# Kernel tuning notes

Measured on AMD Instinct MI355X. Metric: run time of the kernel, lower is better.

## Reference

```python
import jax, jax.numpy as jnp
import numpy as np

IN_DIM = 128
HID = 128
OUT = 128

def _linear(x, W, b):
    return x @ W + b

def setup_inputs() -> dict:
    key = jax.random.key(0)
    ks = jax.random.split(key, 16)
    B, N = 2, 512
    def w(k, fan_in, fan_out):
        lim = 1.0 / np.sqrt(fan_in)
        return jax.random.uniform(k, (fan_in, fan_out), jnp.float32, -lim, lim)
    def bvec(k, fan_in, fan_out):
        lim = 1.0 / np.sqrt(fan_in)
        return jax.random.uniform(k, (fan_out,), jnp.float32, -lim, lim)
    return {
        "features": jax.random.normal(ks[0], (B, N, IN_DIM), jnp.float32),
        "coords": jax.random.normal(ks[1], (B, N, 3), jnp.float32),
        "eW1": w(ks[2], 2 * IN_DIM + 1, HID), "eb1": bvec(ks[3], 2 * IN_DIM + 1, HID),
        "eW2": w(ks[4], HID, HID), "eb2": bvec(ks[5], HID, HID),
        "nW1": w(ks[6], IN_DIM + HID, HID), "nb1": bvec(ks[7], IN_DIM + HID, HID),
        "nW2": w(ks[8], HID, OUT), "nb2": bvec(ks[9], HID, OUT),
        "cW1": w(ks[10], HID, HID), "cb1": bvec(ks[11], HID, HID),
        "cW2": w(ks[12], HID, 1), "cb2": bvec(ks[13], HID, 1),
    }

def reference(features, coords, eW1, eb1, eW2, eb2, nW1, nb1, nW2, nb2, cW1, cb1, cW2, cb2):
    B, N, D = features.shape
    # pairwise coordinate differences and distances: (B, N, N, 3), (B, N, N, 1)
    coord_diff = coords[:, :, None, :] - coords[:, None, :, :]
    distances = jnp.sqrt(jnp.sum(coord_diff ** 2, axis=-1, keepdims=True) + 1e-8)
    # all-pairs edge features: (B, N, N, 2D+1)
    feat_i = jnp.broadcast_to(features[:, :, None, :], (B, N, N, D))
    feat_j = jnp.broadcast_to(features[:, None, :, :], (B, N, N, D))
    edge_features = jnp.concatenate([feat_i, feat_j, distances], axis=-1)
    edge_hidden = _linear(jax.nn.silu(_linear(edge_features, eW1, eb1)), eW2, eb2)
    # mean over neighbors j -> (B, N, HID)
    aggregated = jnp.mean(edge_hidden, axis=2)
    node_input = jnp.concatenate([features, aggregated], axis=-1)
    updated_features = _linear(jax.nn.silu(_linear(node_input, nW1, nb1)), nW2, nb2)
    # coordinate update
    coord_weights = _linear(jax.nn.silu(_linear(edge_hidden, cW1, cb1)), cW2, cb2)  # (B,N,N,1)
    updated_coords = coords + jnp.mean(coord_weights * coord_diff, axis=2)
    return (updated_features, updated_coords)
```

## Files before the change

kernel.cpp:

```cpp
#include <hip/hip_runtime.h>
#include <hip/hip_bf16.h>
#include <math.h>


typedef float f32x4 __attribute__((ext_vector_type(4)));
typedef short short8 __attribute__((ext_vector_type(8)));

#define MFMA16(a, b, c) __builtin_amdgcn_mfma_f32_16x16x32_bf16((a), (b), (c), 0, 0, 0)

__device__ __forceinline__ short f2bf(float x) {
    __hip_bfloat16 h = __float2bfloat16(x);
    union { __hip_bfloat16 h; short s; } v; v.h = h;
    return v.s;
}
__device__ __forceinline__ float bf2f(short s) {
    union { unsigned u; float f; } v; v.u = ((unsigned)(unsigned short)s) << 16;
    return v.f;
}
__device__ __forceinline__ float silu_f(float x) {
    return x * __builtin_amdgcn_rcpf(1.0f + __expf(-x));
}

__device__ __forceinline__ int swz(int row, int col) {
    int byte = (row << 8) | (col << 1);
    byte ^= (row & 7) << 4;
    return byte >> 1;
}

__global__ void egnn_prew(const float* __restrict__ feat, const float* __restrict__ eW1,
                          const float* __restrict__ eb1,
                          const float* __restrict__ eW2, const float* __restrict__ cW1,
                          const float* __restrict__ eb2, const float* __restrict__ cb1,
                          float* __restrict__ Abuf, float* __restrict__ Bbuf,
                          unsigned short* __restrict__ MbfT, float* __restrict__ bias2ws) {
    const int bid = blockIdx.x;
    const int t = threadIdx.x;
    if (bid < 1024) {
        __shared__ float f[128];
        if (t < 128) f[t] = feat[bid * 128 + t];
        __syncthreads();
        const int col  = t & 127;
        const int half = t >> 7;
        const float* W = eW1 + (size_t)half * 128 * 128 + col;
        float acc = half ? 0.f : eb1[col];
        #pragma unroll 8
        for (int k = 0; k < 128; ++k) acc += f[k] * W[(size_t)k * 128];
        if (half == 0) Abuf[bid * 128 + col] = acc;
        else           Bbuf[bid * 128 + col] = acc;
    } else {
        const int idx = (bid - 1024) * 2 + (t >> 7);
        const int c = t & 127;
        if (idx < 128) {
            float acc = 0.f;
            #pragma unroll 8
            for (int h = 0; h < 128; ++h) acc += eW2[idx * 128 + h] * cW1[h * 128 + c];
            MbfT[c * 128 + idx] = (unsigned short)f2bf(acc);
        } else if (idx == 128) {
            float acc = cb1[c];
            #pragma unroll 8
            for (int h = 0; h < 128; ++h) acc += eb2[h] * cW1[h * 128 + c];
            bias2ws[c] = acc;
        }
    }
}

__global__ void __launch_bounds__(512) egnn_main(
    const float* __restrict__ features, const float* __restrict__ coords,
    const float* __restrict__ eW1, const float* __restrict__ eW2,
    const float* __restrict__ eb2,
    const float* __restrict__ nW1, const float* __restrict__ nb1,
    const float* __restrict__ nW2, const float* __restrict__ nb2,
    const float* __restrict__ cW2, const float* __restrict__ cb2,
    const float* __restrict__ Abuf, const float* __restrict__ Bbuf,
    const unsigned short* __restrict__ MbfT, const float* __restrict__ bias2ws,
    float* __restrict__ out_feat, float* __restrict__ out_coord)
{
    constexpr int Nn = 512;
    __shared__ __align__(16) short se[128 * 128];
    __shared__ __align__(16) float dynbuf[1792];
    __shared__ float aw[128], wd[128];
    __shared__ float aggs[128], aggh[128], hbuf[128];
    __shared__ float cred[8][3];
    __shared__ float ci3[3];

    float (*cdp)[3][128]  = reinterpret_cast<float(*)[3][128]>(dynbuf);
    float (*warr)[4][128] = reinterpret_cast<float(*)[4][128]>(dynbuf + 768);
    float (*aggred)[128]  = reinterpret_cast<float(*)[128]>(se);
    float (*part)[128]    = reinterpret_cast<float(*)[128]>(dynbuf);
    float* pfi = dynbuf + 512;

    const int tid  = threadIdx.x;
    const int lane = tid & 63;
    const int wave = tid >> 6;
    const int node = blockIdx.x;
    const int b    = node >> 9;

    if (tid < 128) {
        aw[tid] = Abuf[node * 128 + tid];
        wd[tid] = eW1[256 * 128 + tid];
    }
    if (tid == 0) {
        ci3[0] = coords[node * 3 + 0];
        ci3[1] = coords[node * 3 + 1];
        ci3[2] = coords[node * 3 + 2];
    }

    const int r0 = (wave >> 2) * 64;
    const int c0 = (wave & 3) * 32;
    const int cfrag = c0 + (lane & 15);
    const int koff  = (lane >> 4) * 8;

    short8 wfM[2][4];
    #pragma unroll
    for (int n2 = 0; n2 < 2; ++n2)
        #pragma unroll
        for (int k = 0; k < 4; ++k)
            wfM[n2][k] = *(const short8*)&MbfT[(size_t)(cfrag + n2 * 16) * 128 + k * 32 + koff];
    __syncthreads();

    const float b2_0  = bias2ws[cfrag], b2_1 = bias2ws[cfrag + 16];
    const float cw2_0 = cW2[cfrag],     cw2_1 = cW2[cfrag + 16];
    const float cb2v  = cb2[0];
    const float cix = ci3[0], ciy = ci3[1], ciz = ci3[2];

    const int jr = tid >> 2, cb = (tid & 3) * 32;
    const int rg = tid >> 4, c8 = (tid & 15) * 8;

    float ap[8];
    #pragma unroll
    for (int q = 0; q < 8; ++q) ap[q] = 0.f;
    float cax = 0.f, cay = 0.f, caz = 0.f;

    for (int t = 0; t < 4; ++t) {
        const int par = t & 1;
        {
            const int j = t * 128 + jr;
            const float dx = cix - coords[(b * Nn + j) * 3 + 0];
            const float dy = ciy - coords[(b * Nn + j) * 3 + 1];
            const float dz = ciz - coords[(b * Nn + j) * 3 + 2];
            const float dj = sqrtf(dx * dx + dy * dy + dz * dz + 1e-8f);
            if ((tid & 3) == 0) {
                cdp[par][0][jr] = dx; cdp[par][1][jr] = dy; cdp[par][2][jr] = dz;
            }
            const float* Bj = Bbuf + (size_t)(b * Nn + j) * 128 + cb;
            #pragma unroll
            for (int cc = 0; cc < 32; cc += 8) {
                f32x4 x0 = *(const f32x4*)(Bj + cc);
                f32x4 x1 = *(const f32x4*)(Bj + cc + 4);
                short8 v;
                #pragma unroll
                for (int r = 0; r < 4; ++r) {
                    const int c = cb + cc + r;
                    v[r] = f2bf(silu_f(aw[c] + x0[r] + dj * wd[c]));
                }
                #pragma unroll
                for (int r = 0; r < 4; ++r) {
                    const int c = cb + cc + 4 + r;
                    v[4 + r] = f2bf(silu_f(aw[c] + x1[r] + dj * wd[c]));
                }
                *(short8*)&se[swz(jr, cb + cc)] = v;
            }
        }
        __syncthreads();

        f32x4 acc[4][2];
        #pragma unroll
        for (int m = 0; m < 4; ++m) {
            acc[m][0] = (f32x4){b2_0, b2_0, b2_0, b2_0};
            acc[m][1] = (f32x4){b2_1, b2_1, b2_1, b2_1};
        }
        #pragma unroll
        for (int m = 0; m < 4; ++m)
            #pragma unroll
            for (int k = 0; k < 4; ++k) {
                short8 a = *(const short8*)&se[swz(r0 + m * 16 + (lane & 15), k * 32 + koff)];
                acc[m][0] = MFMA16(a, wfM[0][k], acc[m][0]);
                acc[m][1] = MFMA16(a, wfM[1][k], acc[m][1]);
            }

        #pragma unroll
        for (int r = 0; r < 4; ++r) {
            short8 v = *(const short8*)&se[swz(rg * 4 + r, c8)];
            #pragma unroll
            for (int q = 0; q < 8; ++q) ap[q] += bf2f(v[q]);
        }

        #pragma unroll
        for (int m = 0; m < 4; ++m)
            #pragma unroll
            for (int reg = 0; reg < 4; ++reg) {
                float v = silu_f(acc[m][0][reg]) * cw2_0
                        + silu_f(acc[m][1][reg]) * cw2_1;
                v += __shfl_xor(v, 1); v += __shfl_xor(v, 2);
                v += __shfl_xor(v, 4); v += __shfl_xor(v, 8);
                if ((lane & 15) == 0)
                    warr[par][wave & 3][r0 + m * 16 + (lane >> 4) * 4 + reg] = v;
            }
        __syncthreads();

        if (lane < 16) {
            const int row = wave * 16 + lane;
            const float w = warr[par][0][row] + warr[par][1][row]
                          + warr[par][2][row] + warr[par][3][row] + cb2v;
            cax += w * cdp[par][0][row];
            cay += w * cdp[par][1][row];
            caz += w * cdp[par][2][row];
        }
    }

    #pragma unroll
    for (int q = 0; q < 8; ++q) aggred[rg][c8 + q] = ap[q];
    {
        float sx = cax, sy = cay, sz = caz;
        sx += __shfl_xor(sx, 1); sy += __shfl_xor(sy, 1); sz += __shfl_xor(sz, 1);
        sx += __shfl_xor(sx, 2); sy += __shfl_xor(sy, 2); sz += __shfl_xor(sz, 2);
        sx += __shfl_xor(sx, 4); sy += __shfl_xor(sy, 4); sz += __shfl_xor(sz, 4);
        sx += __shfl_xor(sx, 8); sy += __shfl_xor(sy, 8); sz += __shfl_xor(sz, 8);
        if (lane == 0) { cred[wave][0] = sx; cred[wave][1] = sy; cred[wave][2] = sz; }
    }
    __syncthreads();

    const int c = tid & 127, g = tid >> 7;
    if (tid < 128) {
        float s = 0.f;
        #pragma unroll
        for (int gg = 0; gg < 32; ++gg) s += aggred[gg][tid];
        aggs[tid] = s;
        pfi[tid]  = features[node * 128 + tid];
    }
    if (tid < 3) {
        float s = 0.f;
        #pragma unroll
        for (int w = 0; w < 8; ++w) s += cred[w][tid];
        out_coord[node * 3 + tid] = ci3[tid] + s * (1.f / 512.f);
    }
    __syncthreads();

    {
        float a2 = 0.f;
        #pragma unroll 8
        for (int k = g * 32; k < g * 32 + 32; ++k) a2 += aggs[k] * eW2[k * 128 + c];
        if (g) part[g][c] = a2;
        __syncthreads();
        if (!g) aggh[c] = (a2 + part[1][c] + part[2][c] + part[3][c]) * (1.f / 512.f) + eb2[c];
        __syncthreads();
    }
    {
        float a2 = (g == 0) ? nb1[c] : 0.f;
        if (g < 2) {
            #pragma unroll 8
            for (int k = g * 64; k < g * 64 + 64; ++k) a2 += pfi[k] * nW1[k * 128 + c];
        } else {
            #pragma unroll 8
            for (int k = (g - 2) * 64; k < (g - 2) * 64 + 64; ++k)
                a2 += aggh[k] * nW1[(128 + k) * 128 + c];
        }
        if (g) part[g][c] = a2;
        __syncthreads();
        if (!g) hbuf[c] = silu_f(a2 + part[1][c] + part[2][c] + part[3][c]);
        __syncthreads();
    }
    {
        float a2 = (g == 0) ? nb2[c] : 0.f;
        #pragma unroll 8
        for (int k = g * 32; k < g * 32 + 32; ++k) a2 += hbuf[k] * nW2[k * 128 + c];
        if (g) part[g][c] = a2;
        __syncthreads();
        if (!g) out_feat[node * 128 + c] = a2 + part[1][c] + part[2][c] + part[3][c];
    }
}

extern "C" void kernel_launch(void* const* d_in, const int* in_sizes, int n_in,
                              void* d_out, int out_size, void* d_ws, size_t ws_size,
                              hipStream_t stream)
{
    const float* features = (const float*)d_in[0];
    const float* coords   = (const float*)d_in[1];
    const float* eW1 = (const float*)d_in[2];
    const float* eb1 = (const float*)d_in[3];
    const float* eW2 = (const float*)d_in[4];
    const float* eb2 = (const float*)d_in[5];
    const float* nW1 = (const float*)d_in[6];
    const float* nb1 = (const float*)d_in[7];
    const float* nW2 = (const float*)d_in[8];
    const float* nb2 = (const float*)d_in[9];
    const float* cW1 = (const float*)d_in[10];
    const float* cb1 = (const float*)d_in[11];
    const float* cW2 = (const float*)d_in[12];
    const float* cb2 = (const float*)d_in[13];

    float* out = (float*)d_out;
    float* out_feat  = out;
    float* out_coord = out + 2 * 512 * 128;

    float* Abuf      = (float*)d_ws;
    float* Bbuf      = Abuf + 2 * 512 * 128;
    unsigned short* MbfT = (unsigned short*)(Bbuf + 2 * 512 * 128);
    float* bias2ws   = (float*)(MbfT + 128 * 128);

    egnn_prew<<<1089, 256, 0, stream>>>(features, eW1, eb1, eW2, cW1, eb2, cb1,
                                        Abuf, Bbuf, MbfT, bias2ws);
    egnn_main<<<1024, 512, 0, stream>>>(features, coords, eW1, eW2, eb2,
                                        nW1, nb1, nW2, nb2, cW2, cb2,
                                        Abuf, Bbuf, MbfT, bias2ws,
                                        out_feat, out_coord);
}
```

Measured before the change: 214.2 us.

## Halve main kernel block to 256 threads with 64-row tiles and DPP reductions

Shrinks the main kernel from 512 to 256 threads per node, processing neighbors in eight 64-row tiles instead of four 128-row tiles, which roughly halves shared memory and sets launch bounds for two blocks per CU. Each wave now owns a 32-column slice of the MFMA over all 64 rows. Cross-lane row reductions use DPP and ds_swizzle in place of shuffles, and aw/wd are read as vectors. The tail node MLP is split across 2 groups instead of 4. The cost is twice as many barriers per node and less parallelism in the tail matvecs.

```diff
diff --git a/kernel.cpp b/kernel.cpp
--- a/kernel.cpp
+++ b/kernel.cpp
@@ -64,7 +64,7 @@
     }
 }
 
-__global__ void __launch_bounds__(512) egnn_main(
+__global__ void __launch_bounds__(256, 2) egnn_mainpost(
     const float* __restrict__ features, const float* __restrict__ coords,
     const float* __restrict__ eW1, const float* __restrict__ eW2,
     const float* __restrict__ eb2,
@@ -76,18 +76,15 @@
     float* __restrict__ out_feat, float* __restrict__ out_coord)
 {
     constexpr int Nn = 512;
-    __shared__ __align__(16) short se[128 * 128];
-    __shared__ __align__(16) float dynbuf[1792];
-    __shared__ float aw[128], wd[128];
-    __shared__ float aggs[128], aggh[128], hbuf[128];
-    __shared__ float cred[8][3];
+    __shared__ __align__(16) short se[64 * 128];
+    __shared__ float aw[128], wd[128], pfi[128];
+    __shared__ float cdp[2][3][64];
+    __shared__ float warr[4][64];
+    __shared__ float aggs[128], aggh[128], hbuf[128], part2[128];
+    __shared__ float cred[4][3];
     __shared__ float ci3[3];
 
-    float (*cdp)[3][128]  = reinterpret_cast<float(*)[3][128]>(dynbuf);
-    float (*warr)[4][128] = reinterpret_cast<float(*)[4][128]>(dynbuf + 768);
-    float (*aggred)[128]  = reinterpret_cast<float(*)[128]>(se);
-    float (*part)[128]    = reinterpret_cast<float(*)[128]>(dynbuf);
-    float* pfi = dynbuf + 512;
+    float (*aggred)[128] = reinterpret_cast<float(*)[128]>(se);
 
     const int tid  = threadIdx.x;
     const int lane = tid & 63;
@@ -96,8 +93,9 @@
     const int b    = node >> 9;
 
     if (tid < 128) {
-        aw[tid] = Abuf[node * 128 + tid];
-        wd[tid] = eW1[256 * 128 + tid];
+        aw[tid]  = Abuf[node * 128 + tid];
+        wd[tid]  = eW1[256 * 128 + tid];
+        pfi[tid] = features[node * 128 + tid];
     }
     if (tid == 0) {
         ci3[0] = coords[node * 3 + 0];
@@ -105,11 +103,8 @@
         ci3[2] = coords[node * 3 + 2];
     }
 
-    const int r0 = (wave >> 2) * 64;
-    const int c0 = (wave & 3) * 32;
-    const int cfrag = c0 + (lane & 15);
+    const int cfrag = wave * 32 + (lane & 15);
     const int koff  = (lane >> 4) * 8;
-
     short8 wfM[2][4];
     #pragma unroll
     for (int n2 = 0; n2 < 2; ++n2)
@@ -131,10 +126,10 @@
     for (int q = 0; q < 8; ++q) ap[q] = 0.f;
     float cax = 0.f, cay = 0.f, caz = 0.f;
 
-    for (int t = 0; t < 4; ++t) {
+    for (int t = 0; t < 8; ++t) {
         const int par = t & 1;
         {
-            const int j = t * 128 + jr;
+            const int j = t * 64 + jr;
             const float dx = cix - coords[(b * Nn + j) * 3 + 0];
             const float dy = ciy - coords[(b * Nn + j) * 3 + 1];
             const float dz = ciz - coords[(b * Nn + j) * 3 + 2];
@@ -147,17 +142,15 @@
             for (int cc = 0; cc < 32; cc += 8) {
                 f32x4 x0 = *(const f32x4*)(Bj + cc);
                 f32x4 x1 = *(const f32x4*)(Bj + cc + 4);
+                f32x4 a0 = *(const f32x4*)&aw[cb + cc];
+                f32x4 a1 = *(const f32x4*)&aw[cb + cc + 4];
+                f32x4 w0 = *(const f32x4*)&wd[cb + cc];
+                f32x4 w1 = *(const f32x4*)&wd[cb + cc + 4];
                 short8 v;
                 #pragma unroll
-                for (int r = 0; r < 4; ++r) {
-                    const int c = cb + cc + r;
-                    v[r] = f2bf(silu_f(aw[c] + x0[r] + dj * wd[c]));
-                }
+                for (int r = 0; r < 4; ++r) v[r]     = f2bf(silu_f(a0[r] + x0[r] + dj * w0[r]));
                 #pragma unroll
-                for (int r = 0; r < 4; ++r) {
-                    const int c = cb + cc + 4 + r;
-                    v[4 + r] = f2bf(silu_f(aw[c] + x1[r] + dj * wd[c]));
-                }
+                for (int r = 0; r < 4; ++r) v[4 + r] = f2bf(silu_f(a1[r] + x1[r] + dj * w1[r]));
                 *(short8*)&se[swz(jr, cb + cc)] = v;
             }
         }
@@ -173,7 +166,7 @@
         for (int m = 0; m < 4; ++m)
             #pragma unroll
             for (int k = 0; k < 4; ++k) {
-                short8 a = *(const short8*)&se[swz(r0 + m * 16 + (lane & 15), k * 32 + koff)];
+                short8 a = *(const short8*)&se[swz(m * 16 + (lane & 15), k * 32 + koff)];
                 acc[m][0] = MFMA16(a, wfM[0][k], acc[m][0]);
                 acc[m][1] = MFMA16(a, wfM[1][k], acc[m][1]);
             }
@@ -191,17 +184,20 @@
             for (int reg = 0; reg < 4; ++reg) {
                 float v = silu_f(acc[m][0][reg]) * cw2_0
                         + silu_f(acc[m][1][reg]) * cw2_1;
-                v += __shfl_xor(v, 1); v += __shfl_xor(v, 2);
-                v += __shfl_xor(v, 4); v += __shfl_xor(v, 8);
+                union { float f; int i; } u, o;
+                u.f = v; o.i = __builtin_amdgcn_mov_dpp(u.i, 0xB1, 0xF, 0xF, true); v += o.f;
+                u.f = v; o.i = __builtin_amdgcn_mov_dpp(u.i, 0x4E, 0xF, 0xF, true); v += o.f;
+                u.f = v; o.i = __builtin_amdgcn_ds_swizzle(u.i, 0x101F);            v += o.f;
+                u.f = v; o.i = __builtin_amdgcn_ds_swizzle(u.i, 0x201F);            v += o.f;
                 if ((lane & 15) == 0)
-                    warr[par][wave & 3][r0 + m * 16 + (lane >> 4) * 4 + reg] = v;
+                    warr[wave][m * 16 + (lane >> 4) * 4 + reg] = v;
             }
         __syncthreads();
 
         if (lane < 16) {
             const int row = wave * 16 + lane;
-            const float w = warr[par][0][row] + warr[par][1][row]
-                          + warr[par][2][row] + warr[par][3][row] + cb2v;
+            const float w = warr[0][row] + warr[1][row]
+                          + warr[2][row] + warr[3][row] + cb2v;
             cax += w * cdp[par][0][row];
             cay += w * cdp[par][1][row];
             caz += w * cdp[par][2][row];
@@ -224,49 +220,42 @@
     if (tid < 128) {
         float s = 0.f;
         #pragma unroll
-        for (int gg = 0; gg < 32; ++gg) s += aggred[gg][tid];
+        for (int gg = 0; gg < 16; ++gg) s += aggred[gg][tid];
         aggs[tid] = s;
-        pfi[tid]  = features[node * 128 + tid];
     }
     if (tid < 3) {
-        float s = 0.f;
-        #pragma unroll
-        for (int w = 0; w < 8; ++w) s += cred[w][tid];
-        out_coord[node * 3 + tid] = ci3[tid] + s * (1.f / 512.f);
+        out_coord[node * 3 + tid] = ci3[tid]
+            + (cred[0][tid] + cred[1][tid] + cred[2][tid] + cred[3][tid]) * (1.f / 512.f);
     }
     __syncthreads();
 
     {
         float a2 = 0.f;
         #pragma unroll 8
-        for (int k = g * 32; k < g * 32 + 32; ++k) a2 += aggs[k] * eW2[k * 128 + c];
-        if (g) part[g][c] = a2;
-        __syncthreads();
-        if (!g) aggh[c] = (a2 + part[1][c] + part[2][c] + part[3][c]) * (1.f / 512.f) + eb2[c];
+        for (int k = g * 64; k < g * 64 + 64; ++k) a2 += aggs[k] * eW2[k * 128 + c];
+        if (g == 1) part2[c] = a2;
+        __syncthreads();
+        if (g == 0) aggh[c] = (a2 + part2[c]) * (1.f / 512.f) + eb2[c];
         __syncthreads();
     }
     {
         float a2 = (g == 0) ? nb1[c] : 0.f;
-        if (g < 2) {
-            #pragma unroll 8
-            for (int k = g * 64; k < g * 64 + 64; ++k) a2 += pfi[k] * nW1[k * 128 + c];
-        } else {
-            #pragma unroll 8
-            for (int k = (g - 2) * 64; k < (g - 2) * 64 + 64; ++k)
-                a2 += aggh[k] * nW1[(128 + k) * 128 + c];
-        }
-        if (g) part[g][c] = a2;
-        __syncthreads();
-        if (!g) hbuf[c] = silu_f(a2 + part[1][c] + part[2][c] + part[3][c]);
+        const float* src = (g == 0) ? pfi : aggh;
+        const float* W = nW1 + (size_t)(g << 7) * 128 + c;
+        #pragma unroll 8
+        for (int k = 0; k < 128; ++k) a2 += src[k] * W[(size_t)k * 128];
+        if (g == 1) part2[c] = a2;
+        __syncthreads();
+        if (g == 0) hbuf[c] = silu_f(a2 + part2[c]);
         __syncthreads();
     }
     {
         float a2 = (g == 0) ? nb2[c] : 0.f;
         #pragma unroll 8
-        for (int k = g * 32; k < g * 32 + 32; ++k) a2 += hbuf[k] * nW2[k * 128 + c];
-        if (g) part[g][c] = a2;
-        __syncthreads();
-        if (!g) out_feat[node * 128 + c] = a2 + part[1][c] + part[2][c] + part[3][c];
+        for (int k = g * 64; k < g * 64 + 64; ++k) a2 += hbuf[k] * nW2[k * 128 + c];
+        if (g == 1) part2[c] = a2;
+        __syncthreads();
+        if (g == 0) out_feat[node * 128 + c] = a2 + part2[c];
     }
 }
 
@@ -300,8 +289,8 @@
 
     egnn_prew<<<1089, 256, 0, stream>>>(features, eW1, eb1, eW2, cW1, eb2, cb1,
                                         Abuf, Bbuf, MbfT, bias2ws);
-    egnn_main<<<1024, 512, 0, stream>>>(features, coords, eW1, eW2, eb2,
-                                        nW1, nb1, nW2, nb2, cW2, cb2,
-                                        Abuf, Bbuf, MbfT, bias2ws,
-                                        out_feat, out_coord);
-}
+    egnn_mainpost<<<1024, 256, 0, stream>>>(features, coords, eW1, eW2, eb2,
+                                            nW1, nb1, nW2, nb2, cW2, cb2,
+                                            Abuf, Bbuf, MbfT, bias2ws,
+                                            out_feat, out_coord);
+}
```

Measured after the change: 178.2 us. -16.8%, faster.
